# Optimization experiments

Measured on AMD Instinct MI355X. Metric: run time of the kernel, lower is better.

Reference implementation:

```python
import jax, jax.numpy as jnp
import numpy as np

N_NODES = 100000
HIDDEN = 128
IN_FEAT = 128
N_EDGES = 600000


def setup_inputs() -> dict:
    key = jax.random.key(0)
    ks = jax.random.split(key, 8)
    x = jax.random.normal(ks[0], (N_NODES, IN_FEAT), dtype=jnp.float32)
    edge_index = jax.random.randint(ks[1], (2, N_EDGES), 0, N_NODES, dtype=jnp.int64)
    # Glorot-style init for the three GCNConv layers (in->hidden, hidden->hidden, hidden->hidden)
    s_in = 1.0 / np.sqrt(IN_FEAT)
    s_h = 1.0 / np.sqrt(HIDDEN)
    W1 = jax.random.normal(ks[2], (IN_FEAT, HIDDEN), dtype=jnp.float32) * s_in
    b1 = jnp.zeros((HIDDEN,), dtype=jnp.float32)
    W2 = jax.random.normal(ks[3], (HIDDEN, HIDDEN), dtype=jnp.float32) * s_h
    b2 = jnp.zeros((HIDDEN,), dtype=jnp.float32)
    W3 = jax.random.normal(ks[4], (HIDDEN, HIDDEN), dtype=jnp.float32) * s_h
    b3 = jnp.zeros((HIDDEN,), dtype=jnp.float32)
    return {"x": x, "W1": W1, "b1": b1, "W2": W2, "b2": b2, "W3": W3, "b3": b3,
            "edge_index": edge_index}


def _gcn_conv(x, W, b, row, col, norm, n_nodes):
    # GCNConv (add_self_loops=False): out = D^{-1/2} A D^{-1/2} (x W) + b
    h = x @ W                                   # [N, H]
    msg = h[row] * norm[:, None]                # gather sources, scale per edge [E, H]
    agg = jax.ops.segment_sum(msg, col, num_segments=n_nodes)  # scatter-add to targets
    return agg + b


def reference(x, W1, b1, W2, b2, W3, b3, edge_index):
    row, col = edge_index[0], edge_index[1]
    # Symmetric GCN normalization, no self loops, unit edge weights.
    deg = jax.ops.segment_sum(jnp.ones(row.shape[0], dtype=x.dtype), col,
                              num_segments=N_NODES)
    deg_inv_sqrt = jnp.where(deg > 0, jax.lax.rsqrt(jnp.maximum(deg, 1.0)), 0.0)
    norm = deg_inv_sqrt[row] * deg_inv_sqrt[col]  # [E]

    h = _gcn_conv(x, W1, b1, row, col, norm, N_NODES)
    h = jax.nn.relu(h)  # dropout(p=0.1) is identity in eval mode
    h = _gcn_conv(h, W2, b2, row, col, norm, N_NODES)
    h = jax.nn.relu(h)
    h = _gcn_conv(h, W3, b3, row, col, norm, N_NODES)
    return h
```

## Files before the change

### kernel.cpp

```cpp
#include <hip/hip_runtime.h>
#include <cstddef>

#define NN 100000
#define NE 600000
#define HID 128

typedef _Float16 half8 __attribute__((ext_vector_type(8)));
typedef _Float16 half2t __attribute__((ext_vector_type(2)));
typedef float f32x4 __attribute__((ext_vector_type(4)));

union H8 { _Float16 h[8]; uint4 u; half8 v; };

__global__ void k_degi(const int* __restrict__ col, int* __restrict__ degi, int E) {
    int e = blockIdx.x * blockDim.x + threadIdx.x;
    if (e < E) atomicAdd(&degi[col[e]], 1);
}

__global__ void k_dinv(const int* __restrict__ degi, float* __restrict__ dinv, int N) {
    int i = blockIdx.x * blockDim.x + threadIdx.x;
    if (i < N) {
        int d = degi[i];
        dinv[i] = d > 0 ? rsqrtf((float)d) : 0.0f;
    }
}

__global__ void k_wprep(const float* __restrict__ W1, const float* __restrict__ W2,
                        const float* __restrict__ W3, _Float16* __restrict__ wt) {
    int b = blockIdx.x;
    int layer = b >> 7, k = b & 127;
    const float* W = layer == 0 ? W1 : (layer == 1 ? W2 : W3);
    int c = threadIdx.x;
    wt[((size_t)layer << 14) + c * 128 + k] = (_Float16)W[k * 128 + c];
}

__global__ void k_blocksum(const int* __restrict__ degi, int* __restrict__ bsum, int N) {
    __shared__ int sh[256];
    int i = blockIdx.x * 256 + threadIdx.x;
    sh[threadIdx.x] = i < N ? degi[i] : 0;
    __syncthreads();
    for (int s = 128; s > 0; s >>= 1) {
        if (threadIdx.x < s) sh[threadIdx.x] += sh[threadIdx.x + s];
        __syncthreads();
    }
    if (threadIdx.x == 0) bsum[blockIdx.x] = sh[0];
}

__global__ void k_scan_bsum(int* __restrict__ bsum, int nb) {
    __shared__ int sh[512];
    int tid = threadIdx.x;
    int v = (tid < nb) ? bsum[tid] : 0;
    sh[tid] = v;
    __syncthreads();
    #pragma unroll
    for (int s = 1; s < 512; s <<= 1) {
        int t = (tid >= s) ? sh[tid - s] : 0;
        __syncthreads();
        sh[tid] += t;
        __syncthreads();
    }
    if (tid < nb) bsum[tid] = sh[tid] - v;
}

__global__ void k_scan_apply(const int* __restrict__ degi, const int* __restrict__ bsum,
                             int* __restrict__ rowptr, int* __restrict__ cursor, int N) {
    __shared__ int sh[256];
    int i = blockIdx.x * 256 + threadIdx.x;
    int v = (i < N) ? degi[i] : 0;
    sh[threadIdx.x] = v;
    __syncthreads();
    #pragma unroll
    for (int s = 1; s < 256; s <<= 1) {
        int t = (threadIdx.x >= s) ? sh[threadIdx.x - s] : 0;
        __syncthreads();
        sh[threadIdx.x] += t;
        __syncthreads();
    }
    if (i < N) {
        int excl = bsum[blockIdx.x] + sh[threadIdx.x] - v;
        rowptr[i] = excl;
        cursor[i] = excl;
        if (i == N - 1) rowptr[N] = bsum[blockIdx.x] + sh[threadIdx.x];
    }
}

__global__ void k_fill_csr(const int* __restrict__ row, const int* __restrict__ col,
                           int* __restrict__ cursor, int* __restrict__ csr_src, int E) {
    int e = blockIdx.x * blockDim.x + threadIdx.x;
    if (e >= E) return;
    int r = row[e], c = col[e];
    int pos = atomicAdd(&cursor[c], 1);
    csr_src[pos] = r;
}

template <typename TA>
__global__ __launch_bounds__(256, 2) void k_gemm(
    const TA* __restrict__ A, const _Float16* __restrict__ WT,
    const float* __restrict__ bias, const float* __restrict__ dinv,
    _Float16* __restrict__ H, int nrows)
{
    __shared__ _Float16 asl[128 * 128];
    __shared__ _Float16 wsl[128 * 128];
    const int tid  = threadIdx.x;
    const int lane = tid & 63;
    const int w    = tid >> 6;
    const int wm   = w >> 1, wn = w & 1;
    const int ln15 = lane & 15;
    const int hi   = lane >> 4;
    const int row0 = blockIdx.x * 128;

    #pragma unroll
    for (int i = 0; i < 8; ++i) {
        int g = i * 256 + tid;
        int c = g >> 4, k8 = (g & 15) << 3;
        uint4 wv = *(const uint4*)(WT + c * 128 + k8);
        *(uint4*)&wsl[c * 128 + (k8 ^ ((c & 7) << 3))] = wv;
    }
    #pragma unroll
    for (int i = 0; i < 8; ++i) {
        int g = i * 256 + tid;
        int r = g >> 4, c8 = (g & 15) << 3;
        int gr = row0 + r; if (gr >= nrows) gr = nrows - 1;
        float vf[8];
        if constexpr (sizeof(TA) == 4) {
            const float4* src = (const float4*)(A + (size_t)gr * HID + c8);
            float4 v0 = src[0], v1 = src[1];
            vf[0] = v0.x; vf[1] = v0.y; vf[2] = v0.z; vf[3] = v0.w;
            vf[4] = v1.x; vf[5] = v1.y; vf[6] = v1.z; vf[7] = v1.w;
        } else {
            H8 hv; hv.u = *(const uint4*)(A + (size_t)gr * HID + c8);
            #pragma unroll
            for (int j = 0; j < 8; ++j) vf[j] = (float)hv.h[j];
        }
        if (bias) {
            #pragma unroll
            for (int j = 0; j < 8; ++j) vf[j] = fmaxf(vf[j] + bias[c8 + j], 0.0f);
        }
        H8 o;
        #pragma unroll
        for (int j = 0; j < 8; ++j) o.h[j] = (_Float16)vf[j];
        *(uint4*)&asl[r * 128 + (c8 ^ ((r & 7) << 3))] = o.u;
    }
    __syncthreads();

    f32x4 acc[4][4];
    #pragma unroll
    for (int i = 0; i < 4; ++i)
        #pragma unroll
        for (int j = 0; j < 4; ++j) {
            acc[i][j][0] = 0.0f; acc[i][j][1] = 0.0f;
            acc[i][j][2] = 0.0f; acc[i][j][3] = 0.0f;
        }

    #pragma unroll
    for (int ks = 0; ks < 4; ++ks) {
        const int k0 = ks * 32 + hi * 8;
        half8 a[4], b[4];
        #pragma unroll
        for (int i = 0; i < 4; ++i) {
            int ra = wm * 64 + i * 16 + ln15;
            a[i] = *(const half8*)&asl[ra * 128 + (k0 ^ ((ra & 7) << 3))];
            int cb = wn * 64 + i * 16 + ln15;
            b[i] = *(const half8*)&wsl[cb * 128 + (k0 ^ ((cb & 7) << 3))];
        }
        #pragma unroll
        for (int i = 0; i < 4; ++i)
            #pragma unroll
            for (int j = 0; j < 4; ++j)
                acc[i][j] = __builtin_amdgcn_mfma_f32_16x16x32_f16(a[i], b[j], acc[i][j], 0, 0, 0);
    }

    #pragma unroll
    for (int i = 0; i < 4; ++i) {
        #pragma unroll
        for (int q = 0; q < 4; ++q) {
            int r = row0 + wm * 64 + i * 16 + hi * 4 + q;
            if (r < nrows) {
                float s = dinv[r];
                #pragma unroll
                for (int j = 0; j < 4; ++j) {
                    H[(size_t)r * HID + wn * 64 + j * 16 + ln15] =
                        (_Float16)(acc[i][j][q] * s);
                }
            }
        }
    }
}

template <bool FINAL>
__global__ __launch_bounds__(256) void k_aggregate(
    const _Float16* __restrict__ hs, const int* __restrict__ csr_src,
    const int* __restrict__ rowptr, const float* __restrict__ dinv,
    const float* __restrict__ bias, void* __restrict__ aggv, int N)
{
    int node = blockIdx.x * 4 + (threadIdx.x >> 6);
    if (node >= N) return;
    int lane = threadIdx.x & 63;
    int beg = rowptr[node], end = rowptr[node + 1];
    float accx = 0.0f, accy = 0.0f;
    int i = beg;
    for (; i + 1 < end; i += 2) {
        int s0 = csr_src[i], s1 = csr_src[i + 1];
        half2t v0 = *(const half2t*)(hs + (size_t)s0 * HID + lane * 2);
        half2t v1 = *(const half2t*)(hs + (size_t)s1 * HID + lane * 2);
        accx += (float)v0[0] + (float)v1[0];
        accy += (float)v0[1] + (float)v1[1];
    }
    if (i < end) {
        int s0 = csr_src[i];
        half2t v0 = *(const half2t*)(hs + (size_t)s0 * HID + lane * 2);
        accx += (float)v0[0]; accy += (float)v0[1];
    }
    float s = dinv[node];
    accx *= s; accy *= s;
    if constexpr (FINAL) {
        float2 bv = *(const float2*)(bias + lane * 2);
        float2* dst = (float2*)((float*)aggv + (size_t)node * HID + lane * 2);
        *dst = make_float2(accx + bv.x, accy + bv.y);
    } else {
        half2t o; o[0] = (_Float16)accx; o[1] = (_Float16)accy;
        *(half2t*)((_Float16*)aggv + (size_t)node * HID + lane * 2) = o;
    }
}

extern "C" void kernel_launch(void* const* d_in, const int* in_sizes, int n_in,
                              void* d_out, int out_size, void* d_ws, size_t ws_size,
                              hipStream_t stream)
{
    const float* x  = (const float*)d_in[0];
    const float* W1 = (const float*)d_in[1];
    const float* b1 = (const float*)d_in[2];
    const float* W2 = (const float*)d_in[3];
    const float* b2 = (const float*)d_in[4];
    const float* W3 = (const float*)d_in[5];
    const float* b3 = (const float*)d_in[6];
    const int*   ei = (const int*)d_in[7];
    const int* row  = ei;
    const int* colv = ei + NE;
    float* out = (float*)d_out;

    _Float16* h16 = (_Float16*)d_ws;
    _Float16* a16 = h16 + (size_t)NN * HID;
    _Float16* wt  = a16 + (size_t)NN * HID;
    int*   degi    = (int*)(wt + 3 * 128 * 128);
    float* dinv    = (float*)(degi + NN);
    int*   rowptr  = (int*)(dinv + NN);
    int*   cursor  = rowptr + NN + 1;
    int*   bsum    = cursor + NN;
    int*   csr_src = bsum + 512;

    const int TB = 256;
    const int nScanBlocks = (NN + 255) / 256;

    k_wprep<<<384, 128, 0, stream>>>(W1, W2, W3, wt);
    hipMemsetAsync(degi, 0, NN * sizeof(int), stream);
    k_degi      <<<(NE + TB - 1) / TB, TB, 0, stream>>>(colv, degi, NE);
    k_dinv      <<<(NN + TB - 1) / TB, TB, 0, stream>>>(degi, dinv, NN);
    k_blocksum  <<<nScanBlocks, 256, 0, stream>>>(degi, bsum, NN);
    k_scan_bsum <<<1, 512, 0, stream>>>(bsum, nScanBlocks);
    k_scan_apply<<<nScanBlocks, 256, 0, stream>>>(degi, bsum, rowptr, cursor, NN);
    k_fill_csr  <<<(NE + TB - 1) / TB, TB, 0, stream>>>(row, colv, cursor, csr_src, NE);

    const int gemmBlocks = (NN + 127) / 128;
    const int aggBlocks  = (NN + 3) / 4;

    k_gemm<float><<<gemmBlocks, TB, 0, stream>>>(x, wt, nullptr, dinv, h16, NN);
    k_aggregate<false><<<aggBlocks, TB, 0, stream>>>(h16, csr_src, rowptr, dinv, nullptr, a16, NN);
    k_gemm<_Float16><<<gemmBlocks, TB, 0, stream>>>(a16, wt + (1 << 14), b1, dinv, h16, NN);
    k_aggregate<false><<<aggBlocks, TB, 0, stream>>>(h16, csr_src, rowptr, dinv, nullptr, a16, NN);
    k_gemm<_Float16><<<gemmBlocks, TB, 0, stream>>>(a16, wt + (2 << 14), b2, dinv, h16, NN);
    k_aggregate<true><<<aggBlocks, TB, 0, stream>>>(h16, csr_src, rowptr, dinv, b3, out, NN);
}
```

Baseline: 289.9 us.

## Widen aggregate gathers to 16-byte loads and fuse bias+relu into aggregation

The aggregate kernel now splits each wavefront into four edge slots of 16 lanes, each lane loading 8 halves (16 bytes) per edge, then reduces across slots with shuffles. This cuts per-edge memory transactions and raises memory-level parallelism. Bias add and ReLU move from the GEMM A-load into the aggregate epilogue, so the fp16 GEMM path becomes a plain copy into shared memory. The dinv kernel is folded into the blocksum kernel, which removes one launch. The cost is more shuffle work and idle lanes for low-degree nodes.

```diff
diff --git a/kernel.cpp b/kernel.cpp
--- a/kernel.cpp
+++ b/kernel.cpp
@@ -6,7 +6,6 @@
 #define HID 128
 
 typedef _Float16 half8 __attribute__((ext_vector_type(8)));
-typedef _Float16 half2t __attribute__((ext_vector_type(2)));
 typedef float f32x4 __attribute__((ext_vector_type(4)));
 
 union H8 { _Float16 h[8]; uint4 u; half8 v; };
@@ -14,14 +13,6 @@
 __global__ void k_degi(const int* __restrict__ col, int* __restrict__ degi, int E) {
     int e = blockIdx.x * blockDim.x + threadIdx.x;
     if (e < E) atomicAdd(&degi[col[e]], 1);
-}
-
-__global__ void k_dinv(const int* __restrict__ degi, float* __restrict__ dinv, int N) {
-    int i = blockIdx.x * blockDim.x + threadIdx.x;
-    if (i < N) {
-        int d = degi[i];
-        dinv[i] = d > 0 ? rsqrtf((float)d) : 0.0f;
-    }
 }
 
 __global__ void k_wprep(const float* __restrict__ W1, const float* __restrict__ W2,
@@ -33,10 +24,13 @@
     wt[((size_t)layer << 14) + c * 128 + k] = (_Float16)W[k * 128 + c];
 }
 
-__global__ void k_blocksum(const int* __restrict__ degi, int* __restrict__ bsum, int N) {
+__global__ void k_blocksum(const int* __restrict__ degi, float* __restrict__ dinv,
+                           int* __restrict__ bsum, int N) {
     __shared__ int sh[256];
     int i = blockIdx.x * 256 + threadIdx.x;
-    sh[threadIdx.x] = i < N ? degi[i] : 0;
+    int v = i < N ? degi[i] : 0;
+    if (i < N) dinv[i] = v > 0 ? rsqrtf((float)v) : 0.0f;
+    sh[threadIdx.x] = v;
     __syncthreads();
     for (int s = 128; s > 0; s >>= 1) {
         if (threadIdx.x < s) sh[threadIdx.x] += sh[threadIdx.x + s];
@@ -95,8 +89,7 @@
 template <typename TA>
 __global__ __launch_bounds__(256, 2) void k_gemm(
     const TA* __restrict__ A, const _Float16* __restrict__ WT,
-    const float* __restrict__ bias, const float* __restrict__ dinv,
-    _Float16* __restrict__ H, int nrows)
+    const float* __restrict__ dinv, _Float16* __restrict__ H, int nrows)
 {
     __shared__ _Float16 asl[128 * 128];
     __shared__ _Float16 wsl[128 * 128];
@@ -120,25 +113,19 @@
         int g = i * 256 + tid;
         int r = g >> 4, c8 = (g & 15) << 3;
         int gr = row0 + r; if (gr >= nrows) gr = nrows - 1;
-        float vf[8];
         if constexpr (sizeof(TA) == 4) {
             const float4* src = (const float4*)(A + (size_t)gr * HID + c8);
             float4 v0 = src[0], v1 = src[1];
-            vf[0] = v0.x; vf[1] = v0.y; vf[2] = v0.z; vf[3] = v0.w;
-            vf[4] = v1.x; vf[5] = v1.y; vf[6] = v1.z; vf[7] = v1.w;
+            H8 o;
+            o.h[0] = (_Float16)v0.x; o.h[1] = (_Float16)v0.y;
+            o.h[2] = (_Float16)v0.z; o.h[3] = (_Float16)v0.w;
+            o.h[4] = (_Float16)v1.x; o.h[5] = (_Float16)v1.y;
+            o.h[6] = (_Float16)v1.z; o.h[7] = (_Float16)v1.w;
+            *(uint4*)&asl[r * 128 + (c8 ^ ((r & 7) << 3))] = o.u;
         } else {
-            H8 hv; hv.u = *(const uint4*)(A + (size_t)gr * HID + c8);
-            #pragma unroll
-            for (int j = 0; j < 8; ++j) vf[j] = (float)hv.h[j];
-        }
-        if (bias) {
-            #pragma unroll
-            for (int j = 0; j < 8; ++j) vf[j] = fmaxf(vf[j] + bias[c8 + j], 0.0f);
-        }
-        H8 o;
-        #pragma unroll
-        for (int j = 0; j < 8; ++j) o.h[j] = (_Float16)vf[j];
-        *(uint4*)&asl[r * 128 + (c8 ^ ((r & 7) << 3))] = o.u;
+            uint4 u = *(const uint4*)(A + (size_t)gr * HID + c8);
+            *(uint4*)&asl[r * 128 + (c8 ^ ((r & 7) << 3))] = u;
+        }
     }
     __syncthreads();
 
@@ -186,7 +173,7 @@
     }
 }
 
-template <bool FINAL>
+template <int MODE>
 __global__ __launch_bounds__(256) void k_aggregate(
     const _Float16* __restrict__ hs, const int* __restrict__ csr_src,
     const int* __restrict__ rowptr, const float* __restrict__ dinv,
@@ -194,31 +181,63 @@
 {
     int node = blockIdx.x * 4 + (threadIdx.x >> 6);
     if (node >= N) return;
-    int lane = threadIdx.x & 63;
+    int lane  = threadIdx.x & 63;
+    int eslot = lane >> 4;
+    int fg    = lane & 15;
     int beg = rowptr[node], end = rowptr[node + 1];
-    float accx = 0.0f, accy = 0.0f;
-    int i = beg;
-    for (; i + 1 < end; i += 2) {
-        int s0 = csr_src[i], s1 = csr_src[i + 1];
-        half2t v0 = *(const half2t*)(hs + (size_t)s0 * HID + lane * 2);
-        half2t v1 = *(const half2t*)(hs + (size_t)s1 * HID + lane * 2);
-        accx += (float)v0[0] + (float)v1[0];
-        accy += (float)v0[1] + (float)v1[1];
-    }
-    if (i < end) {
-        int s0 = csr_src[i];
-        half2t v0 = *(const half2t*)(hs + (size_t)s0 * HID + lane * 2);
-        accx += (float)v0[0]; accy += (float)v0[1];
-    }
-    float s = dinv[node];
-    accx *= s; accy *= s;
-    if constexpr (FINAL) {
-        float2 bv = *(const float2*)(bias + lane * 2);
-        float2* dst = (float2*)((float*)aggv + (size_t)node * HID + lane * 2);
-        *dst = make_float2(accx + bv.x, accy + bv.y);
-    } else {
-        half2t o; o[0] = (_Float16)accx; o[1] = (_Float16)accy;
-        *(half2t*)((_Float16*)aggv + (size_t)node * HID + lane * 2) = o;
+
+    float accf[8];
+    #pragma unroll
+    for (int j = 0; j < 8; ++j) accf[j] = 0.0f;
+
+    const uint4 z = make_uint4(0, 0, 0, 0);
+    int nr = (end - beg + 3) >> 2;
+    int e  = beg + eslot;
+    int r  = 0;
+    for (; r + 1 < nr; r += 2, e += 8) {
+        int s0 = (e     < end) ? csr_src[e]     : -1;
+        int s1 = (e + 4 < end) ? csr_src[e + 4] : -1;
+        uint4 u0 = (s0 >= 0) ? *(const uint4*)(hs + (size_t)s0 * HID + fg * 8) : z;
+        uint4 u1 = (s1 >= 0) ? *(const uint4*)(hs + (size_t)s1 * HID + fg * 8) : z;
+        H8 h0; h0.u = u0;
+        H8 h1; h1.u = u1;
+        #pragma unroll
+        for (int j = 0; j < 8; ++j)
+            accf[j] += (float)h0.h[j] + (float)h1.h[j];
+    }
+    if (r < nr) {
+        int s0 = (e < end) ? csr_src[e] : -1;
+        uint4 u0 = (s0 >= 0) ? *(const uint4*)(hs + (size_t)s0 * HID + fg * 8) : z;
+        H8 h0; h0.u = u0;
+        #pragma unroll
+        for (int j = 0; j < 8; ++j) accf[j] += (float)h0.h[j];
+    }
+
+    #pragma unroll
+    for (int j = 0; j < 8; ++j) {
+        accf[j] += __shfl_xor(accf[j], 16);
+        accf[j] += __shfl_xor(accf[j], 32);
+    }
+
+    if (eslot == 0) {
+        float s = dinv[node];
+        float4 b0 = *(const float4*)(bias + fg * 8);
+        float4 b1 = *(const float4*)(bias + fg * 8 + 4);
+        float o[8];
+        o[0] = accf[0] * s + b0.x; o[1] = accf[1] * s + b0.y;
+        o[2] = accf[2] * s + b0.z; o[3] = accf[3] * s + b0.w;
+        o[4] = accf[4] * s + b1.x; o[5] = accf[5] * s + b1.y;
+        o[6] = accf[6] * s + b1.z; o[7] = accf[7] * s + b1.w;
+        if constexpr (MODE == 0) {
+            H8 oh;
+            #pragma unroll
+            for (int j = 0; j < 8; ++j) oh.h[j] = (_Float16)fmaxf(o[j], 0.0f);
+            *(uint4*)((_Float16*)aggv + (size_t)node * HID + fg * 8) = oh.u;
+        } else {
+            float* dst = (float*)aggv + (size_t)node * HID + fg * 8;
+            *(float4*)dst       = make_float4(o[0], o[1], o[2], o[3]);
+            *(float4*)(dst + 4) = make_float4(o[4], o[5], o[6], o[7]);
+        }
     }
 }
 
@@ -254,8 +273,7 @@
     k_wprep<<<384, 128, 0, stream>>>(W1, W2, W3, wt);
     hipMemsetAsync(degi, 0, NN * sizeof(int), stream);
     k_degi      <<<(NE + TB - 1) / TB, TB, 0, stream>>>(colv, degi, NE);
-    k_dinv      <<<(NN + TB - 1) / TB, TB, 0, stream>>>(degi, dinv, NN);
-    k_blocksum  <<<nScanBlocks, 256, 0, stream>>>(degi, bsum, NN);
+    k_blocksum  <<<nScanBlocks, 256, 0, stream>>>(degi, dinv, bsum, NN);
     k_scan_bsum <<<1, 512, 0, stream>>>(bsum, nScanBlocks);
     k_scan_apply<<<nScanBlocks, 256, 0, stream>>>(degi, bsum, rowptr, cursor, NN);
     k_fill_csr  <<<(NE + TB - 1) / TB, TB, 0, stream>>>(row, colv, cursor, csr_src, NE);
@@ -263,10 +281,10 @@
     const int gemmBlocks = (NN + 127) / 128;
     const int aggBlocks  = (NN + 3) / 4;
 
-    k_gemm<float><<<gemmBlocks, TB, 0, stream>>>(x, wt, nullptr, dinv, h16, NN);
-    k_aggregate<false><<<aggBlocks, TB, 0, stream>>>(h16, csr_src, rowptr, dinv, nullptr, a16, NN);
-    k_gemm<_Float16><<<gemmBlocks, TB, 0, stream>>>(a16, wt + (1 << 14), b1, dinv, h16, NN);
-    k_aggregate<false><<<aggBlocks, TB, 0, stream>>>(h16, csr_src, rowptr, dinv, nullptr, a16, NN);
-    k_gemm<_Float16><<<gemmBlocks, TB, 0, stream>>>(a16, wt + (2 << 14), b2, dinv, h16, NN);
-    k_aggregate<true><<<aggBlocks, TB, 0, stream>>>(h16, csr_src, rowptr, dinv, b3, out, NN);
-}
+    k_gemm<float><<<gemmBlocks, TB, 0, stream>>>(x, wt, dinv, h16, NN);
+    k_aggregate<0><<<aggBlocks, TB, 0, stream>>>(h16, csr_src, rowptr, dinv, b1, a16, NN);
+    k_gemm<_Float16><<<gemmBlocks, TB, 0, stream>>>(a16, wt + (1 << 14), dinv, h16, NN);
+    k_aggregate<0><<<aggBlocks, TB, 0, stream>>>(h16, csr_src, rowptr, dinv, b2, a16, NN);
+    k_gemm<_Float16><<<gemmBlocks, TB, 0, stream>>>(a16, wt + (2 << 14), dinv, h16, NN);
+    k_aggregate<1><<<aggBlocks, TB, 0, stream>>>(h16, csr_src, rowptr, dinv, b3, out, NN);
+}
```

Result: faster. 256.0 us (-11.7%).
